# Performance work log

Hardware: AMD Instinct MI355X
Metric: run time of the kernel (lower is better)

The kernel has to match this reference:

```python
import jax, jax.numpy as jnp
import numpy as np

RADIUS = 0.2
NSAMPLE = 32
BANDWIDTH = 0.1


def ellipsoid_query(xyz, new_xyz, radius, nsample):
    """xyz:(B,N,3), new_xyz:(B,P,3) -> idx:(B,P,nsample) int32.
    Ellipsoid semi-axes (radius, 2*radius, radius); first nsample hits,
    padded with the first hit (index 0 if empty), matching the CUDA kernel.
    """
    B, N, _ = xyz.shape
    inv_sq = jnp.asarray([1.0 / radius**2, 1.0 / (2.0 * radius) ** 2, 1.0 / radius**2],
                         dtype=xyz.dtype)
    # accumulate per-coordinate to avoid a (B,P,N,3) intermediate
    q = jnp.zeros((B, new_xyz.shape[1], N), dtype=xyz.dtype)
    for k in range(3):
        d = new_xyz[:, :, None, k] - xyz[:, None, :, k]  # (B,P,N)
        q = q + d * d * inv_sq[k]
    mask = q < 1.0
    cand = jnp.where(mask, jnp.arange(N, dtype=jnp.int32), jnp.int32(N))  # invalid -> N
    cand = jnp.sort(cand, axis=-1)[..., :nsample]                          # (B,P,S)
    first = cand[..., :1]
    first = jnp.where(first >= N, jnp.int32(0), first)
    return jnp.where(cand >= N, first, cand)


def group(features, idx):
    """features:(B,C,N), idx:(B,P,S) -> (B,C,P,S)"""
    return jnp.take_along_axis(features[:, :, None, :], idx[:, None, :, :], axis=-1)


def setup_inputs() -> dict:
    key = jax.random.key(0)
    k1, k2, k3 = jax.random.split(key, 3)
    xyz = jax.random.uniform(k1, (4, 8192, 3), dtype=jnp.float32)
    new_xyz = jax.random.uniform(k2, (4, 2048, 3), dtype=jnp.float32)
    features = jax.random.normal(k3, (4, 64, 8192), dtype=jnp.float32)
    return {"xyz": xyz, "new_xyz": new_xyz, "features": features}


def reference(xyz, new_xyz, features):
    idx = ellipsoid_query(xyz, new_xyz, RADIUS, NSAMPLE)          # (B,P,S)
    xyz_trans = jnp.transpose(xyz, (0, 2, 1))                      # (B,3,N)
    grouped_xyz = group(xyz_trans, idx)                            # (B,3,P,S)
    # density: gaussian of distance to center
    g = jnp.transpose(grouped_xyz, (0, 2, 3, 1))                   # (B,P,S,3)
    dist = jnp.linalg.norm(g - new_xyz[:, :, None, :], axis=-1)    # (B,P,S)
    density = jnp.exp(-dist**2 / (2.0 * BANDWIDTH**2)) / (2.5 * BANDWIDTH)
    grouped_density = (1.0 / density)[:, None, :, :]               # (B,1,P,S)
    grouped_features = group(features, idx)                        # (B,C,P,S)
    return jnp.concatenate([grouped_xyz, grouped_density, grouped_features], axis=1)
```

## Files before the change

kernel.cpp:

```cpp
#include <hip/hip_runtime.h>

constexpr int NPTS = 8192;
constexpr int NQ   = 2048;
constexpr int NC   = 64;
constexpr int NS   = 32;
constexpr int NCH  = 3 + 1 + NC;
constexpr int CS   = NQ * NS;
constexpr int LPTS = 5120;
constexpr int QPB2 = 16;



struct ScanLds { float pts[3][LPTS]; int idx[QPB2][NS]; };
union  KLds    { ScanLds s; float tile[2][NC][65]; };

__device__ __forceinline__ unsigned prefix_popc(unsigned long long m) {
    return __builtin_amdgcn_mbcnt_hi((unsigned)(m >> 32),
           __builtin_amdgcn_mbcnt_lo((unsigned)m, 0u));
}

__global__ __launch_bounds__(1024, 8) void scan_trans_kernel(
    const float* __restrict__ xyz,
    const float* __restrict__ nxyz,
    const float* __restrict__ feat,
    float* __restrict__ ftr,
    int* __restrict__ gidx,
    float* __restrict__ out,
    int ntrans)
{
    __shared__ KLds u;
    const int bx = blockIdx.x;
    const int t  = threadIdx.x;

    if (bx < ntrans) {
        const int b   = bx >> 6;
        const int tl2 = bx & 63;
        const int h   = t >> 9;
        const int v   = t & 511;
        const int pl  = v & 63;
        const int c0  = v >> 6;
        const int n0  = tl2 * 128 + h * 64;
        const float* fb = feat + (size_t)b * NC * NPTS;
        #pragma unroll
        for (int i = 0; i < 8; ++i) {
            const int c = c0 + 8 * i;
            u.tile[h][c][pl] = fb[(size_t)c * NPTS + n0 + pl];
        }
        __syncthreads();
        float* tb = ftr + ((size_t)b * NPTS + n0) * NC;
        #pragma unroll
        for (int i = 0; i < 8; ++i) {
            const int pp = c0 + 8 * i;
            tb[(size_t)pp * NC + pl] = u.tile[h][pl][pp];
        }
        return;
    }

    const int sb   = bx - ntrans;
    const int qpb  = NQ / QPB2;
    const int b    = sb / qpb;
    const int p0   = (sb - b * qpb) * QPB2;
    const int lane = t & 63;
    const int wave = t >> 6;
    const float* xb = xyz + (size_t)b * NPTS * 3;

    #pragma unroll
    for (int k = 0; k < 3 * LPTS / 1024; ++k) {
        const int g  = k * 1024 + t;
        const float val = xb[g];
        const int pt = g / 3;
        const int c  = g - 3 * pt;
        u.s.pts[c][pt] = val;
    }
    __syncthreads();

    const int p = p0 + wave;
    const float qx = nxyz[((size_t)b * NQ + p) * 3 + 0];
    const float qy = nxyz[((size_t)b * NQ + p) * 3 + 1];
    const float qz = nxyz[((size_t)b * NQ + p) * 3 + 2];

    int cnt = 0;
    int first = -1;
    int* idx_row = u.s.idx[wave];

    for (int base = 0; base < LPTS; base += 128) {
        const int i0 = base + lane;
        const int i1 = i0 + 64;
        const float xA = u.s.pts[0][i0];
        const float xB = u.s.pts[0][i1];
        const float yA = u.s.pts[1][i0];
        const float yB = u.s.pts[1][i1];
        const float zA = u.s.pts[2][i0];
        const float zB = u.s.pts[2][i1];

        const float dxA = __fsub_rn(qx, xA);
        const float dyA = __fsub_rn(qy, yA);
        const float dzA = __fsub_rn(qz, zA);
        const float qA  = __fadd_rn(__fadd_rn(
                            __fmul_rn(__fmul_rn(dxA, dxA), 25.0f),
                            __fmul_rn(__fmul_rn(dyA, dyA), 6.25f)),
                            __fmul_rn(__fmul_rn(dzA, dzA), 25.0f));
        const float dxB = __fsub_rn(qx, xB);
        const float dyB = __fsub_rn(qy, yB);
        const float dzB = __fsub_rn(qz, zB);
        const float qB  = __fadd_rn(__fadd_rn(
                            __fmul_rn(__fmul_rn(dxB, dxB), 25.0f),
                            __fmul_rn(__fmul_rn(dyB, dyB), 6.25f)),
                            __fmul_rn(__fmul_rn(dzB, dzB), 25.0f));
        const bool hitA = qA < 1.0f;
        const bool hitB = qB < 1.0f;

        const unsigned long long m0 = __ballot(hitA);
        const unsigned long long m1 = __ballot(hitB);
        if (first < 0) {
            if (m0 != 0ull)      first = base + __builtin_ctzll(m0);
            else if (m1 != 0ull) first = base + 64 + __builtin_ctzll(m1);
        }
        if (hitA) {
            const int pos = cnt + (int)prefix_popc(m0);
            if (pos < NS) idx_row[pos] = i0;
        }
        const int c0 = __popcll(m0);
        if (hitB) {
            const int pos = cnt + c0 + (int)prefix_popc(m1);
            if (pos < NS) idx_row[pos] = i1;
        }
        cnt += c0 + __popcll(m1);
        if (cnt >= NS) break;
    }

    if (cnt < NS) {
        float x0 = xb[3 * (LPTS + lane) + 0];
        float y0 = xb[3 * (LPTS + lane) + 1];
        float z0 = xb[3 * (LPTS + lane) + 2];
        float x1 = xb[3 * (LPTS + 64 + lane) + 0];
        float y1 = xb[3 * (LPTS + 64 + lane) + 1];
        float z1 = xb[3 * (LPTS + 64 + lane) + 2];
        for (int base = LPTS; base < NPTS; base += 64) {
            float xn = 0.f, yn = 0.f, zn = 0.f;
            const int pf = base + 128;
            if (pf < NPTS) {
                xn = xb[3 * (pf + lane) + 0];
                yn = xb[3 * (pf + lane) + 1];
                zn = xb[3 * (pf + lane) + 2];
            }
            const float dx = __fsub_rn(qx, x0);
            const float dy = __fsub_rn(qy, y0);
            const float dz = __fsub_rn(qz, z0);
            const float t0 = __fmul_rn(__fmul_rn(dx, dx), 25.0f);
            const float t1 = __fmul_rn(__fmul_rn(dy, dy), 6.25f);
            const float t2 = __fmul_rn(__fmul_rn(dz, dz), 25.0f);
            const float qv = __fadd_rn(__fadd_rn(t0, t1), t2);
            const bool hit = qv < 1.0f;

            const unsigned long long m = __ballot(hit);
            if (first < 0 && m != 0ull)
                first = base + __builtin_ctzll(m);
            if (hit) {
                const int pos = cnt + (int)prefix_popc(m);
                if (pos < NS) idx_row[pos] = base + lane;
            }
            cnt += __popcll(m);
            if (cnt >= NS) break;
            x0 = x1; y0 = y1; z0 = z1;
            x1 = xn; y1 = yn; z1 = zn;
        }
    }

    if (cnt < NS) {
        const int f = (cnt == 0) ? 0 : first;
        if (lane < NS && lane >= cnt) idx_row[lane] = f;
    }

    if (lane < NS) {
        const int s = lane;
        const int j = idx_row[s];
        gidx[((size_t)b * NQ + p) * NS + s] = j;

        const float px = xb[3 * j + 0];
        const float py = xb[3 * j + 1];
        const float pz = xb[3 * j + 2];
        const float dx = __fsub_rn(px, qx);
        const float dy = __fsub_rn(py, qy);
        const float dz = __fsub_rn(pz, qz);
        const float d2 = __fadd_rn(__fadd_rn(__fmul_rn(dx, dx), __fmul_rn(dy, dy)),
                                   __fmul_rn(dz, dz));
        const float dist = __fsqrt_rn(d2);
        const float arg  = __fdiv_rn(-__fmul_rn(dist, dist), 0.02f);
        const float density = __fmul_rn(expf(arg), 4.0f);
        const float gd = __fdiv_rn(1.0f, density);

        float* ob = out + ((size_t)b * NCH * NQ + p) * NS + s;
        ob[0 * (size_t)CS] = px;
        ob[1 * (size_t)CS] = py;
        ob[2 * (size_t)CS] = pz;
        ob[3 * (size_t)CS] = gd;
    }
}

__global__ __launch_bounds__(512, 8) void group_kernel(
    const int* __restrict__ gidx,
    const float* __restrict__ ftr,
    float* __restrict__ out,
    int B)
{
    __shared__ float ldsc[NC][33];

    const int g = blockIdx.x;
    int b, p;
    if (B == 4) {
        b = (g & 7) >> 1;
        p = ((g >> 3) << 1) | (g & 1);
    } else {
        b = g / NQ;
        p = g - b * NQ;
    }
    const int tid = threadIdx.x;

    const int cg = tid & 15;
    const int sl = tid >> 4;
    const int j  = gidx[((size_t)b * NQ + p) * NS + sl];
    const float4 v = ((const float4*)(ftr + ((size_t)b * NPTS + j) * NC))[cg];
    ldsc[4 * cg + 0][sl] = v.x;
    ldsc[4 * cg + 1][sl] = v.y;
    ldsc[4 * cg + 2][sl] = v.z;
    ldsc[4 * cg + 3][sl] = v.w;
    __syncthreads();

    const int c  = tid >> 3;
    const int s4 = (tid & 7) << 2;
    float4 w;
    w.x = ldsc[c][s4 + 0];
    w.y = ldsc[c][s4 + 1];
    w.z = ldsc[c][s4 + 2];
    w.w = ldsc[c][s4 + 3];
    float* op = out + (((size_t)b * NCH + 4 + c) * NQ + p) * NS + s4;
    *(float4*)op = w;
}

__global__ __launch_bounds__(512, 8) void ellip_direct_kernel(
    const float* __restrict__ xyz,
    const float* __restrict__ nxyz,
    const float* __restrict__ feat,
    float* __restrict__ out)
{
    __shared__ int idx_s[8][NS];

    const int b    = blockIdx.y;
    const int p0   = blockIdx.x * 8;
    const int tid  = threadIdx.x;
    const int lane = tid & 63;
    const int wave = tid >> 6;
    const float* xb = xyz + (size_t)b * NPTS * 3;

    {
        const int p = p0 + wave;
        const float qx = nxyz[((size_t)b * NQ + p) * 3 + 0];
        const float qy = nxyz[((size_t)b * NQ + p) * 3 + 1];
        const float qz = nxyz[((size_t)b * NQ + p) * 3 + 2];
        int cnt = 0, first = -1;
        for (int base = 0; base < NPTS; base += 64) {
            const int i = base + lane;
            const float dx = __fsub_rn(qx, xb[i * 3 + 0]);
            const float dy = __fsub_rn(qy, xb[i * 3 + 1]);
            const float dz = __fsub_rn(qz, xb[i * 3 + 2]);
            const float t0 = __fmul_rn(__fmul_rn(dx, dx), 25.0f);
            const float t1 = __fmul_rn(__fmul_rn(dy, dy), 6.25f);
            const float t2 = __fmul_rn(__fmul_rn(dz, dz), 25.0f);
            const float qv = __fadd_rn(__fadd_rn(t0, t1), t2);
            const bool hit = qv < 1.0f;
            const unsigned long long m = __ballot(hit);
            if (first < 0 && m != 0ull) first = base + __builtin_ctzll(m);
            if (hit) {
                const int pos = cnt + __popcll(m & ((1ull << lane) - 1ull));
                if (pos < NS) idx_s[wave][pos] = i;
            }
            cnt += __popcll(m);
            if (cnt >= NS) break;
        }
        if (cnt < NS) {
            const int f = (cnt == 0) ? 0 : first;
            if (lane < NS && lane >= cnt) idx_s[wave][lane] = f;
        }
    }
    __syncthreads();

    const int s = tid & 31;
    const int h = (tid >> 5) & 1;
    const int q = tid >> 6;
    const int p = p0 + q;
    const int j = idx_s[q][s];
    float* ob = out + ((size_t)b * NCH * NQ + p) * NS + s;

    if (h == 0) {
        const float qx = nxyz[((size_t)b * NQ + p) * 3 + 0];
        const float qy = nxyz[((size_t)b * NQ + p) * 3 + 1];
        const float qz = nxyz[((size_t)b * NQ + p) * 3 + 2];
        const float px = xb[j * 3 + 0], py = xb[j * 3 + 1], pz = xb[j * 3 + 2];
        const float dx = __fsub_rn(px, qx);
        const float dy = __fsub_rn(py, qy);
        const float dz = __fsub_rn(pz, qz);
        const float d2 = __fadd_rn(__fadd_rn(__fmul_rn(dx, dx), __fmul_rn(dy, dy)),
                                   __fmul_rn(dz, dz));
        const float dist = __fsqrt_rn(d2);
        const float arg  = __fdiv_rn(-__fmul_rn(dist, dist), 0.02f);
        const float gd = __fdiv_rn(1.0f, __fmul_rn(expf(arg), 4.0f));
        ob[0 * (size_t)CS] = px;
        ob[1 * (size_t)CS] = py;
        ob[2 * (size_t)CS] = pz;
        ob[3 * (size_t)CS] = gd;
    }
    const float* fb = feat + (size_t)b * NC * NPTS + j;
    #pragma unroll 4
    for (int c = h; c < NC; c += 2)
        ob[(size_t)(4 + c) * CS] = fb[(size_t)c * NPTS];
}

extern "C" void kernel_launch(void* const* d_in, const int* in_sizes, int n_in,
                              void* d_out, int out_size, void* d_ws, size_t ws_size,
                              hipStream_t stream) {
    const float* xyz  = (const float*)d_in[0];
    const float* nxyz = (const float*)d_in[1];
    const float* feat = (const float*)d_in[2];
    float* out = (float*)d_out;

    const int B = in_sizes[0] / (NPTS * 3);
    const size_t ftr_f = (size_t)B * NPTS * NC;
    const size_t idx_f = (size_t)B * NQ * NS;
    const size_t need  = (ftr_f + idx_f) * 4;

    if (ws_size >= need) {
        float* ftr = (float*)d_ws;
        int*   idx = (int*)(ftr + ftr_f);

        const int ntrans = B * 64;
        const int nscan  = B * (NQ / QPB2);
        scan_trans_kernel<<<dim3(ntrans + nscan), 1024, 0, stream>>>(
            xyz, nxyz, feat, ftr, idx, out, ntrans);
        group_kernel<<<dim3(B * NQ), 512, 0, stream>>>(idx, ftr, out, B);
    } else {
        ellip_direct_kernel<<<dim3(NQ / 8, B), 512, 0, stream>>>(xyz, nxyz, feat, out);
    }
}
```

Baseline: 100.8 us.

## Fuse transpose, scan and grouping into one cooperative kernel with grid sync

Replaces the two-launch path (scan+transpose kernel, then group kernel) with a single cooperative kernel. Each block first transposes a feature tile and writes an SoA copy of xyz, then all blocks meet at a grid-wide sync. After that each block scans 16 queries against the global SoA points (2 per wave) and gathers features from the index rows kept in LDS, so the global index buffer round-trip and the second launch go away. The cost is a grid barrier, only 512 blocks of 512 threads (B*128), scans that read global or L2 memory instead of LDS-staged points, and a fallback to the old path if the cooperative launch fails.

```diff
diff --git a/kernel.cpp b/kernel.cpp
--- a/kernel.cpp
+++ b/kernel.cpp
@@ -1,4 +1,7 @@
 #include <hip/hip_runtime.h>
+#include <hip/hip_cooperative_groups.h>
+
+namespace cg = cooperative_groups;
 
 constexpr int NPTS = 8192;
 constexpr int NQ   = 2048;
@@ -6,27 +9,172 @@
 constexpr int NS   = 32;
 constexpr int NCH  = 3 + 1 + NC;
 constexpr int CS   = NQ * NS;
-constexpr int LPTS = 5120;
-constexpr int QPB2 = 16;
-
-
-
-struct ScanLds { float pts[3][LPTS]; int idx[QPB2][NS]; };
-union  KLds    { ScanLds s; float tile[2][NC][65]; };
+
+
 
 __device__ __forceinline__ unsigned prefix_popc(unsigned long long m) {
     return __builtin_amdgcn_mbcnt_hi((unsigned)(m >> 32),
            __builtin_amdgcn_mbcnt_lo((unsigned)m, 0u));
 }
 
-__global__ __launch_bounds__(1024, 8) void scan_trans_kernel(
+union FusedLds {
+    float tile[NC][65];
+    struct { int idx[16][NS]; float ldsc[NC][33]; } sg;
+};
+
+__global__ __launch_bounds__(512, 4) void fused_kernel(
     const float* __restrict__ xyz,
     const float* __restrict__ nxyz,
     const float* __restrict__ feat,
     float* __restrict__ ftr,
-    int* __restrict__ gidx,
+    float* __restrict__ soa,
     float* __restrict__ out,
-    int ntrans)
+    int B)
+{
+    __shared__ FusedLds u;
+    const int g = blockIdx.x;
+    const int t = threadIdx.x;
+    int b, r;
+    if (B == 4) { b = (g & 7) >> 1; r = ((g >> 3) << 1) | (g & 1); }
+    else        { b = g >> 7;       r = g & 127; }
+
+    const float* xb = xyz + (size_t)b * NPTS * 3;
+    float* xs = soa + (size_t)b * 3 * NPTS;
+    float* ys = xs + NPTS;
+    float* zs = ys + NPTS;
+
+    {
+        const int n0 = r * 64;
+        const float* fb = feat + (size_t)b * NC * NPTS;
+        const int pl = t & 63;
+        const int c0 = t >> 6;
+        #pragma unroll
+        for (int i = 0; i < 8; ++i) {
+            const int c = c0 + 8 * i;
+            u.tile[c][pl] = fb[(size_t)c * NPTS + n0 + pl];
+        }
+        __syncthreads();
+        float* tb = ftr + ((size_t)b * NPTS + n0) * NC;
+        #pragma unroll
+        for (int i = 0; i < 8; ++i) {
+            const int pp = c0 + 8 * i;
+            tb[(size_t)pp * NC + pl] = u.tile[pl][pp];
+        }
+        if (t < 64) {
+            const int i = n0 + t;
+            xs[i] = xb[3 * i + 0];
+            ys[i] = xb[3 * i + 1];
+            zs[i] = xb[3 * i + 2];
+        }
+    }
+    cg::this_grid().sync();
+
+    const int lane = t & 63;
+    const int wave = t >> 6;
+    for (int k = 0; k < 2; ++k) {
+        const int qi = wave * 2 + k;
+        const int p  = r * 16 + qi;
+        int* idx_row = u.sg.idx[qi];
+
+        const float qx = nxyz[((size_t)b * NQ + p) * 3 + 0];
+        const float qy = nxyz[((size_t)b * NQ + p) * 3 + 1];
+        const float qz = nxyz[((size_t)b * NQ + p) * 3 + 2];
+
+        int cnt = 0;
+        int first = -1;
+
+        float x0 = xs[lane],      y0 = ys[lane],      z0 = zs[lane];
+        float x1 = xs[64 + lane], y1 = ys[64 + lane], z1 = zs[64 + lane];
+
+        for (int base = 0; base < NPTS; base += 64) {
+            float xn = 0.f, yn = 0.f, zn = 0.f;
+            const int pf = base + 128;
+            if (pf < NPTS) {
+                xn = xs[pf + lane]; yn = ys[pf + lane]; zn = zs[pf + lane];
+            }
+            const float dx = __fsub_rn(qx, x0);
+            const float dy = __fsub_rn(qy, y0);
+            const float dz = __fsub_rn(qz, z0);
+            const float t0 = __fmul_rn(__fmul_rn(dx, dx), 25.0f);
+            const float t1 = __fmul_rn(__fmul_rn(dy, dy), 6.25f);
+            const float t2 = __fmul_rn(__fmul_rn(dz, dz), 25.0f);
+            const float qv = __fadd_rn(__fadd_rn(t0, t1), t2);
+            const bool hit = qv < 1.0f;
+
+            const unsigned long long m = __ballot(hit);
+            if (first < 0 && m != 0ull)
+                first = base + __builtin_ctzll(m);
+            if (hit) {
+                const int pos = cnt + (int)prefix_popc(m);
+                if (pos < NS) idx_row[pos] = base + lane;
+            }
+            cnt += __popcll(m);
+            if (cnt >= NS) break;
+            x0 = x1; y0 = y1; z0 = z1;
+            x1 = xn; y1 = yn; z1 = zn;
+        }
+        if (cnt < NS) {
+            const int f = (cnt == 0) ? 0 : first;
+            if (lane < NS && lane >= cnt) idx_row[lane] = f;
+        }
+
+        if (lane < NS) {
+            const int s = lane;
+            const int j = idx_row[s];
+            const float px = xs[j], py = ys[j], pz = zs[j];
+            const float dx = __fsub_rn(px, qx);
+            const float dy = __fsub_rn(py, qy);
+            const float dz = __fsub_rn(pz, qz);
+            const float d2 = __fadd_rn(__fadd_rn(__fmul_rn(dx, dx),
+                                                 __fmul_rn(dy, dy)),
+                                       __fmul_rn(dz, dz));
+            const float dist = __fsqrt_rn(d2);
+            const float arg  = __fdiv_rn(-__fmul_rn(dist, dist), 0.02f);
+            const float density = __fmul_rn(expf(arg), 4.0f);
+            const float gd = __fdiv_rn(1.0f, density);
+
+            float* ob = out + ((size_t)b * NCH * NQ + p) * NS + s;
+            ob[0 * (size_t)CS] = px;
+            ob[1 * (size_t)CS] = py;
+            ob[2 * (size_t)CS] = pz;
+            ob[3 * (size_t)CS] = gd;
+        }
+    }
+    __syncthreads();
+
+    const int cgi = t & 15;
+    const int sl  = t >> 4;
+    const int cch = t >> 3;
+    const int s4  = (t & 7) << 2;
+    for (int q = 0; q < 16; ++q) {
+        const int p = r * 16 + q;
+        const int j = u.sg.idx[q][sl];
+        const float4 v = ((const float4*)(ftr + ((size_t)b * NPTS + j) * NC))[cgi];
+        u.sg.ldsc[4 * cgi + 0][sl] = v.x;
+        u.sg.ldsc[4 * cgi + 1][sl] = v.y;
+        u.sg.ldsc[4 * cgi + 2][sl] = v.z;
+        u.sg.ldsc[4 * cgi + 3][sl] = v.w;
+        __syncthreads();
+        float4 w;
+        w.x = u.sg.ldsc[cch][s4 + 0];
+        w.y = u.sg.ldsc[cch][s4 + 1];
+        w.z = u.sg.ldsc[cch][s4 + 2];
+        w.w = u.sg.ldsc[cch][s4 + 3];
+        float* op = out + (((size_t)b * NCH + 4 + cch) * NQ + p) * NS + s4;
+        *(float4*)op = w;
+        __syncthreads();
+    }
+}
+
+constexpr int LPTS = 5120;
+constexpr int QPB2 = 16;
+struct ScanLds { float pts[3][LPTS]; int idx[QPB2][NS]; };
+union  KLds    { ScanLds s; float tile[2][NC][65]; };
+
+__global__ __launch_bounds__(1024, 8) void scan_trans_kernel(
+    const float* __restrict__ xyz, const float* __restrict__ nxyz,
+    const float* __restrict__ feat, float* __restrict__ ftr,
+    int* __restrict__ gidx, float* __restrict__ out, int ntrans)
 {
     __shared__ KLds u;
     const int bx = blockIdx.x;
@@ -79,19 +227,15 @@
     const float qy = nxyz[((size_t)b * NQ + p) * 3 + 1];
     const float qz = nxyz[((size_t)b * NQ + p) * 3 + 2];
 
-    int cnt = 0;
-    int first = -1;
+    int cnt = 0, first = -1;
     int* idx_row = u.s.idx[wave];
 
     for (int base = 0; base < LPTS; base += 128) {
         const int i0 = base + lane;
         const int i1 = i0 + 64;
-        const float xA = u.s.pts[0][i0];
-        const float xB = u.s.pts[0][i1];
-        const float yA = u.s.pts[1][i0];
-        const float yB = u.s.pts[1][i1];
-        const float zA = u.s.pts[2][i0];
-        const float zB = u.s.pts[2][i1];
+        const float xA = u.s.pts[0][i0], xB = u.s.pts[0][i1];
+        const float yA = u.s.pts[1][i0], yB = u.s.pts[1][i1];
+        const float zA = u.s.pts[2][i0], zB = u.s.pts[2][i1];
 
         const float dxA = __fsub_rn(qx, xA);
         const float dyA = __fsub_rn(qy, yA);
@@ -152,10 +296,8 @@
             const float t2 = __fmul_rn(__fmul_rn(dz, dz), 25.0f);
             const float qv = __fadd_rn(__fadd_rn(t0, t1), t2);
             const bool hit = qv < 1.0f;
-
             const unsigned long long m = __ballot(hit);
-            if (first < 0 && m != 0ull)
-                first = base + __builtin_ctzll(m);
+            if (first < 0 && m != 0ull) first = base + __builtin_ctzll(m);
             if (hit) {
                 const int pos = cnt + (int)prefix_popc(m);
                 if (pos < NS) idx_row[pos] = base + lane;
@@ -176,7 +318,6 @@
         const int s = lane;
         const int j = idx_row[s];
         gidx[((size_t)b * NQ + p) * NS + s] = j;
-
         const float px = xb[3 * j + 0];
         const float py = xb[3 * j + 1];
         const float pz = xb[3 * j + 2];
@@ -199,22 +340,14 @@
 }
 
 __global__ __launch_bounds__(512, 8) void group_kernel(
-    const int* __restrict__ gidx,
-    const float* __restrict__ ftr,
-    float* __restrict__ out,
-    int B)
+    const int* __restrict__ gidx, const float* __restrict__ ftr,
+    float* __restrict__ out, int B)
 {
     __shared__ float ldsc[NC][33];
-
     const int g = blockIdx.x;
     int b, p;
-    if (B == 4) {
-        b = (g & 7) >> 1;
-        p = ((g >> 3) << 1) | (g & 1);
-    } else {
-        b = g / NQ;
-        p = g - b * NQ;
-    }
+    if (B == 4) { b = (g & 7) >> 1; p = ((g >> 3) << 1) | (g & 1); }
+    else        { b = g / NQ;       p = g - b * NQ; }
     const int tid = threadIdx.x;
 
     const int cg = tid & 15;
@@ -239,20 +372,16 @@
 }
 
 __global__ __launch_bounds__(512, 8) void ellip_direct_kernel(
-    const float* __restrict__ xyz,
-    const float* __restrict__ nxyz,
-    const float* __restrict__ feat,
-    float* __restrict__ out)
+    const float* __restrict__ xyz, const float* __restrict__ nxyz,
+    const float* __restrict__ feat, float* __restrict__ out)
 {
     __shared__ int idx_s[8][NS];
-
     const int b    = blockIdx.y;
     const int p0   = blockIdx.x * 8;
     const int tid  = threadIdx.x;
     const int lane = tid & 63;
     const int wave = tid >> 6;
     const float* xb = xyz + (size_t)b * NPTS * 3;
-
     {
         const int p = p0 + wave;
         const float qx = nxyz[((size_t)b * NQ + p) * 3 + 0];
@@ -284,14 +413,12 @@
         }
     }
     __syncthreads();
-
     const int s = tid & 31;
     const int h = (tid >> 5) & 1;
     const int q = tid >> 6;
     const int p = p0 + q;
     const int j = idx_s[q][s];
     float* ob = out + ((size_t)b * NCH * NQ + p) * NS + s;
-
     if (h == 0) {
         const float qx = nxyz[((size_t)b * NQ + p) * 3 + 0];
         const float qy = nxyz[((size_t)b * NQ + p) * 3 + 1];
@@ -326,12 +453,22 @@
 
     const int B = in_sizes[0] / (NPTS * 3);
     const size_t ftr_f = (size_t)B * NPTS * NC;
+    const size_t soa_f = (size_t)B * 3 * NPTS;
     const size_t idx_f = (size_t)B * NQ * NS;
-    const size_t need  = (ftr_f + idx_f) * 4;
+    const size_t need  = (ftr_f + soa_f + idx_f) * 4;
 
     if (ws_size >= need) {
         float* ftr = (float*)d_ws;
-        int*   idx = (int*)(ftr + ftr_f);
+        float* soa = ftr + ftr_f;
+        int*   idx = (int*)(soa + soa_f);
+
+        const float* a0 = xyz; const float* a1 = nxyz; const float* a2 = feat;
+        float* a3 = ftr; float* a4 = soa; float* a5 = out; int a6 = B;
+        void* args[] = { &a0, &a1, &a2, &a3, &a4, &a5, &a6 };
+        hipError_t e = hipLaunchCooperativeKernel(
+            (const void*)fused_kernel, dim3(B * 128), dim3(512), args, 0, stream);
+        if (e == hipSuccess) return;
+        (void)hipGetLastError();
 
         const int ntrans = B * 64;
         const int nscan  = B * (NQ / QPB2);
```

Measured after the change: 167.2 us. 1.66x slower.
